# Performance work log

Hardware: AMD Instinct MI355X
Metric: run time of the kernel (lower is better)

Reference implementation:

```python
import jax, jax.numpy as jnp
import numpy as np

N_NODES = 100000
D = 128            # node feature dim == hidden_units[0]
N_EDGES = 640000
BN_EPS = 1e-3      # keras BatchNormalization default epsilon


def setup_inputs() -> dict:
    key = jax.random.key(0)
    ks = jax.random.split(key, 12)
    node_repr = jax.random.normal(ks[0], (N_NODES, D), dtype=jnp.float32)
    edges = jax.random.randint(ks[1], (2, N_EDGES), 0, N_NODES, dtype=jnp.int64)
    # ffn_prepare: BN(D) -> Dense(D, gelu)   (dropout inactive at inference)
    bn1_gamma = jax.random.normal(ks[2], (D,), dtype=jnp.float32) * 0.1 + 1.0
    bn1_beta = jax.random.normal(ks[3], (D,), dtype=jnp.float32) * 0.1
    bn1_mean = jax.random.normal(ks[4], (D,), dtype=jnp.float32) * 0.1
    bn1_var = jax.random.uniform(ks[5], (D,), dtype=jnp.float32) + 0.5
    W1 = jax.random.normal(ks[6], (D, D), dtype=jnp.float32) / np.sqrt(D)
    b1 = jnp.zeros((D,), dtype=jnp.float32)
    # update_fn: BN(2D) -> Dense(D, gelu)
    bn2_gamma = jax.random.normal(ks[7], (2 * D,), dtype=jnp.float32) * 0.1 + 1.0
    bn2_beta = jax.random.normal(ks[8], (2 * D,), dtype=jnp.float32) * 0.1
    bn2_mean = jax.random.normal(ks[9], (2 * D,), dtype=jnp.float32) * 0.1
    bn2_var = jax.random.uniform(ks[10], (2 * D,), dtype=jnp.float32) + 0.5
    W2 = jax.random.normal(ks[11], (2 * D, D), dtype=jnp.float32) / np.sqrt(2 * D)
    b2 = jnp.zeros((D,), dtype=jnp.float32)
    return dict(node_repr=node_repr, edges=edges,
                bn1_gamma=bn1_gamma, bn1_beta=bn1_beta, bn1_mean=bn1_mean, bn1_var=bn1_var,
                W1=W1, b1=b1,
                bn2_gamma=bn2_gamma, bn2_beta=bn2_beta, bn2_mean=bn2_mean, bn2_var=bn2_var,
                W2=W2, b2=b2)


def _bn(x, gamma, beta, mean, var):
    # inference-mode batch norm
    return (x - mean) * jax.lax.rsqrt(var + BN_EPS) * gamma + beta


def reference(node_repr, edges, bn1_gamma, bn1_beta, bn1_mean, bn1_var, W1, b1,
              bn2_gamma, bn2_beta, bn2_mean, bn2_var, W2, b2):
    num_nodes = node_repr.shape[0]
    node_indices, neighbour_indices = edges[0], edges[1]
    # gather neighbour features: [E, D]
    neigh = node_repr[neighbour_indices]
    # prepare FFN (BN -> dropout(identity at eval) -> Dense + exact gelu)
    msg = jax.nn.gelu(_bn(neigh, bn1_gamma, bn1_beta, bn1_mean, bn1_var) @ W1 + b1,
                      approximate=False)
    # unsorted_segment_mean: sum / count, empty segments -> 0 (TF semantics)
    sums = jax.ops.segment_sum(msg, node_indices, num_segments=num_nodes)
    cnt = jax.ops.segment_sum(jnp.ones((edges.shape[1],), msg.dtype), node_indices,
                              num_segments=num_nodes)
    agg = sums / jnp.maximum(cnt, 1.0)[:, None]
    # update FFN on concat [node_repr, agg]: [N, 2D] -> [N, D]
    h = jnp.concatenate([node_repr, agg], axis=1)
    out = jax.nn.gelu(_bn(h, bn2_gamma, bn2_beta, bn2_mean, bn2_var) @ W2 + b2,
                      approximate=False)
    return out
```

## Files before the change

### kernel.cpp

```cpp
#include <hip/hip_runtime.h>

#define NN 100000
#define DD 128
#define EE 640000
#define BN_EPS 1e-3f
#define NBLK 391
#define NTILE 6250
#define EPB 1637
#define FFN1_BLKS 782
#define FFN2_BLKS 768

typedef __bf16 bf16x8 __attribute__((ext_vector_type(8)));
typedef float f32x4 __attribute__((ext_vector_type(4)));

#define W1F_OFF 0u
#define W2F_OFF 32768u
#define B1F_OFF 98304u
#define B2F_OFF 98816u
#define T_OFF   99328u
#define OFFS_OFF 26099328u
#define ELIST_OFF 26899328u
#define CNTG_OFF ELIST_OFF
#define BOFS_OFF (ELIST_OFF + 611524u)
#define BSUM_OFF 29459328u
#define AGG_OFF 29464576u
#define XB_OFF  55064576u

__device__ __forceinline__ float gelu_fast(float x) {
    float x3 = x * x * x;
    float z2 = 1.5957691216057308f * x + 0.07135481627002407f * x3;
    return x / (1.0f + __expf(-z2));
}

__global__ __launch_bounds__(256) void prep_kernel(
    const float* __restrict__ g1, const float* __restrict__ be1,
    const float* __restrict__ m1, const float* __restrict__ v1,
    const float* __restrict__ W1, const float* __restrict__ b1,
    const float* __restrict__ g2, const float* __restrict__ be2,
    const float* __restrict__ m2, const float* __restrict__ v2,
    const float* __restrict__ W2, const float* __restrict__ b2,
    const int* __restrict__ edges,
    __bf16* __restrict__ W1f, __bf16* __restrict__ W2f,
    float* __restrict__ b1f, float* __restrict__ b2f,
    int* __restrict__ cntg)
{
    const int blk = blockIdx.x;
    const int t = threadIdx.x;
    if (blk < 64) {
        const int w = (blk * 256 + t) >> 6;
        const int lane = t & 63;
        if (w < 128) {
            float acc = 0.f;
            for (int k = lane; k < 128; k += 64) {
                float s = g1[k] * rsqrtf(v1[k] + BN_EPS);
                float sh = be1[k] - m1[k] * s;
                acc += sh * W1[k * 128 + w];
            }
#pragma unroll
            for (int off = 32; off > 0; off >>= 1) acc += __shfl_down(acc, off);
            if (lane == 0) b1f[w] = acc + b1[w];
        } else {
            const int n = w - 128;
            float acc = 0.f;
            for (int k = lane; k < 256; k += 64) {
                float s = g2[k] * rsqrtf(v2[k] + BN_EPS);
                float sh = be2[k] - m2[k] * s;
                acc += sh * W2[k * 128 + n];
            }
#pragma unroll
            for (int off = 32; off > 0; off >>= 1) acc += __shfl_down(acc, off);
            if (lane == 0) b2f[n] = acc + b2[n];
        }
    } else if (blk < 256) {
        int tid = (blk - 64) * 256 + t;
        if (tid < 16384) {
            int idx = tid;
            int i = idx & 7, l = (idx >> 3) & 63, nt = (idx >> 9) & 7, kt = idx >> 12;
            int k = kt * 32 + (l >> 4) * 8 + i;
            int n = nt * 16 + (l & 15);
            float s = g1[k] * rsqrtf(v1[k] + BN_EPS);
            W1f[idx] = (__bf16)(s * W1[k * 128 + n]);
        } else {
            int idx = tid - 16384;
            int i = idx & 7, l = (idx >> 3) & 63, nt = (idx >> 9) & 7, kt = idx >> 12;
            int n = nt * 16 + (l & 15);
            int row;
            if (kt < 4) {
                row = kt * 32 + (l >> 4) * 8 + i;
            } else {
                int q = (kt - 4) * 32 + (l >> 4) * 8 + i;
                row = 128 + ((q & 7) * 16 + (q >> 3));
            }
            float s = g2[row] * rsqrtf(v2[row] + BN_EPS);
            W2f[idx] = (__bf16)(s * W2[row * 128 + n]);
        }
    } else {
        __shared__ int cnt[NBLK];
        const int k = blk - 256;
        for (int b = t; b < NBLK; b += 256) cnt[b] = 0;
        __syncthreads();
        const int e0 = k * EPB, e1 = min(e0 + EPB, EE);
        for (int e = e0 + t; e < e1; e += 256)
            atomicAdd(&cnt[edges[e] >> 8], 1);
        __syncthreads();
        for (int b = t; b < NBLK; b += 256) cntg[k * NBLK + b] = cnt[b];
    }
}

__global__ __launch_bounds__(256) void sortb_kernel(const int* __restrict__ cntg,
                                                    int* __restrict__ bofs,
                                                    int* __restrict__ bsum)
{
    const int b = blockIdx.x, t = threadIdx.x;
    __shared__ int sp[256];
    int ia = 2 * t, ib = 2 * t + 1;
    int va = (ia < NBLK) ? cntg[ia * NBLK + b] : 0;
    int vb = (ib < NBLK) ? cntg[ib * NBLK + b] : 0;
    sp[t] = va + vb;
    __syncthreads();
    for (int off = 1; off < 256; off <<= 1) {
        int tmp = (t >= off) ? sp[t - off] : 0;
        __syncthreads();
        sp[t] += tmp;
        __syncthreads();
    }
    int pexcl = sp[t] - (va + vb);
    if (ia < NBLK) bofs[b * NBLK + ia] = pexcl;
    if (ib < NBLK) bofs[b * NBLK + ib] = pexcl + va;
    if (t == 255) bsum[b] = sp[255];
}

__global__ __launch_bounds__(256) void sortc_kernel(const int* __restrict__ edges,
                                                    const int* __restrict__ bsum,
                                                    const int* __restrict__ bofs,
                                                    int* __restrict__ pairbuf)
{
    __shared__ int sp[256];
    __shared__ int cur[NBLK];
    const int k = blockIdx.x, t = threadIdx.x;
    int ia = 2 * t, ib = 2 * t + 1;
    int va = (ia < NBLK) ? bsum[ia] : 0;
    int vb = (ib < NBLK) ? bsum[ib] : 0;
    sp[t] = va + vb;
    __syncthreads();
    for (int off = 1; off < 256; off <<= 1) {
        int tmp = (t >= off) ? sp[t - off] : 0;
        __syncthreads();
        sp[t] += tmp;
        __syncthreads();
    }
    int pexcl = sp[t] - (va + vb);
    if (ia < NBLK) cur[ia] = pexcl + bofs[ia * NBLK + k];
    if (ib < NBLK) cur[ib] = pexcl + va + bofs[ib * NBLK + k];
    __syncthreads();
    const int e0 = k * EPB, e1 = min(e0 + EPB, EE);
    for (int e = e0 + t; e < e1; e += 256) {
        int dst = edges[e];
        int src = edges[EE + e];
        int pos = atomicAdd(&cur[dst >> 8], 1);
        pairbuf[pos] = (src << 8) | (dst & 255);
    }
}

__global__ __launch_bounds__(256) void p2_ffn1_kernel(
    const int* __restrict__ bsum, const int* __restrict__ pairbuf,
    int* __restrict__ elist, int* __restrict__ offs,
    const float* __restrict__ X, const __bf16* __restrict__ W1f,
    const float* __restrict__ b1f, __bf16* __restrict__ T,
    __bf16* __restrict__ Xb)
{
    __shared__ __bf16 sW[16384];
    const int t = threadIdx.x;
    if (blockIdx.x < NBLK) {
        int* sArr = (int*)sW;
        int* cur  = sArr + 256;
        int* red  = sArr + 512;
        const int b = blockIdx.x;
        int part = 0;
        for (int i = t; i < b; i += 256) part += bsum[i];
#pragma unroll
        for (int off = 32; off > 0; off >>= 1) part += __shfl_down(part, off);
        if ((t & 63) == 0) red[t >> 6] = part;
        cur[t] = 0;
        __syncthreads();
        const int start = red[0] + red[1] + red[2] + red[3];
        const int end = start + bsum[b];
        for (int e = start + t; e < end; e += 256)
            atomicAdd(&cur[pairbuf[e] & 255], 1);
        __syncthreads();
        int v = cur[t];
        sArr[t] = v;
        __syncthreads();
        for (int off = 1; off < 256; off <<= 1) {
            int tmp = (t >= off) ? sArr[t - off] : 0;
            __syncthreads();
            sArr[t] += tmp;
            __syncthreads();
        }
        int ex = sArr[t] - v + start;
        const int node = b * 256 + t;
        if (node <= NN) offs[node] = ex;
        __syncthreads();
        cur[t] = ex;
        __syncthreads();
        for (int e = start + t; e < end; e += 256) {
            int item = pairbuf[e];
            int pos = atomicAdd(&cur[item & 255], 1);
            elist[pos] = item >> 8;
        }
        return;
    }
#pragma unroll
    for (int i = 0; i < 8; ++i) {
        int ch = i * 256 + t;
        *(bf16x8*)(sW + ch * 8) = *(const bf16x8*)(W1f + (size_t)ch * 8);
    }
    __syncthreads();

    const int wave = t >> 6;
    const int lane = t & 63;
    const int c = lane & 15, kh = lane >> 4;
    const int tbase = (blockIdx.x - NBLK) * 8;
    const int tile0 = tbase + wave;
    const int tile1 = tbase + 4 + wave;

    float bias[8];
#pragma unroll
    for (int nt = 0; nt < 8; ++nt) bias[nt] = b1f[nt * 16 + c];

    f32x4 r0[4], r1[4], s0[4], s1[4];
    bf16x8 af[4];

    if (tile0 < NTILE) {
        const float* xr = X + (size_t)(tile0 * 16 + c) * DD + kh * 8;
#pragma unroll
        for (int q = 0; q < 4; ++q) {
            r0[q] = *(const f32x4*)(xr + q * 32);
            r1[q] = *(const f32x4*)(xr + q * 32 + 4);
        }
    }
    if (tile1 < NTILE) {
        const float* xr = X + (size_t)(tile1 * 16 + c) * DD + kh * 8;
#pragma unroll
        for (int q = 0; q < 4; ++q) {
            s0[q] = *(const f32x4*)(xr + q * 32);
            s1[q] = *(const f32x4*)(xr + q * 32 + 4);
        }
    }

    if (tile0 < NTILE) {
        const size_t rowb = (size_t)(tile0 * 16 + c) * DD;
#pragma unroll
        for (int kt = 0; kt < 4; ++kt) {
            bf16x8 fa;
#pragma unroll
            for (int i = 0; i < 4; ++i) { fa[i] = (__bf16)r0[kt][i]; fa[4 + i] = (__bf16)r1[kt][i]; }
            af[kt] = fa;
            *(bf16x8*)(Xb + rowb + kt * 32 + kh * 8) = fa;
        }
        f32x4 acc[8] = {};
#pragma unroll
        for (int kt = 0; kt < 4; ++kt)
#pragma unroll
            for (int nt = 0; nt < 8; ++nt) {
                bf16x8 bfr = *(const bf16x8*)(sW + ((kt * 8 + nt) * 64 + lane) * 8);
                acc[nt] = __builtin_amdgcn_mfma_f32_16x16x32_bf16(af[kt], bfr, acc[nt], 0, 0, 0);
            }
#pragma unroll
        for (int r = 0; r < 4; ++r) {
            int row = tile0 * 16 + kh * 4 + r;
            bf16x8 o;
#pragma unroll
            for (int nt = 0; nt < 8; ++nt)
                o[nt] = (__bf16)gelu_fast(acc[nt][r] + bias[nt]);
            *(bf16x8*)(T + (size_t)row * DD + c * 8) = o;
        }
    }
    if (tile1 < NTILE) {
        const size_t rowb = (size_t)(tile1 * 16 + c) * DD;
#pragma unroll
        for (int kt = 0; kt < 4; ++kt) {
            bf16x8 fa;
#pragma unroll
            for (int i = 0; i < 4; ++i) { fa[i] = (__bf16)s0[kt][i]; fa[4 + i] = (__bf16)s1[kt][i]; }
            af[kt] = fa;
            *(bf16x8*)(Xb + rowb + kt * 32 + kh * 8) = fa;
        }
        f32x4 acc[8] = {};
#pragma unroll
        for (int kt = 0; kt < 4; ++kt)
#pragma unroll
            for (int nt = 0; nt < 8; ++nt) {
                bf16x8 bfr = *(const bf16x8*)(sW + ((kt * 8 + nt) * 64 + lane) * 8);
                acc[nt] = __builtin_amdgcn_mfma_f32_16x16x32_bf16(af[kt], bfr, acc[nt], 0, 0, 0);
            }
#pragma unroll
        for (int r = 0; r < 4; ++r) {
            int row = tile1 * 16 + kh * 4 + r;
            bf16x8 o;
#pragma unroll
            for (int nt = 0; nt < 8; ++nt)
                o[nt] = (__bf16)gelu_fast(acc[nt][r] + bias[nt]);
            *(bf16x8*)(T + (size_t)row * DD + c * 8) = o;
        }
    }
}

__global__ __launch_bounds__(256) void agg_kernel(
    const __bf16* __restrict__ T, const int* __restrict__ offs,
    const int* __restrict__ elist, __bf16* __restrict__ Agg)
{
    int t = blockIdx.x * 256 + threadIdx.x;
    int node = t >> 4, j = t & 15;
    if (node >= NN) return;
    const int lane = threadIdx.x & 63;
    const int gbase = lane & 48;
    const int beg = offs[node];
    const int end = offs[node + 1];
    const int d = end - beg;
    float acc[8] = {};
    for (int eb = beg; eb < end; eb += 16) {
        int me = eb + (lane & 15);
        int sv = (me < end) ? elist[me] : 0;
        int cnt = min(end - eb, 16);
        int i = 0;
        for (; i + 3 < cnt; i += 4) {
            int s0 = __shfl(sv, gbase + i);
            int s1 = __shfl(sv, gbase + i + 1);
            int s2 = __shfl(sv, gbase + i + 2);
            int s3 = __shfl(sv, gbase + i + 3);
            bf16x8 v0 = *(const bf16x8*)(T + (size_t)s0 * DD + j * 8);
            bf16x8 v1 = *(const bf16x8*)(T + (size_t)s1 * DD + j * 8);
            bf16x8 v2 = *(const bf16x8*)(T + (size_t)s2 * DD + j * 8);
            bf16x8 v3 = *(const bf16x8*)(T + (size_t)s3 * DD + j * 8);
#pragma unroll
            for (int q = 0; q < 8; ++q)
                acc[q] += ((float)v0[q] + (float)v1[q]) + ((float)v2[q] + (float)v3[q]);
        }
        for (; i < cnt; ++i) {
            int s0 = __shfl(sv, gbase + i);
            bf16x8 v0 = *(const bf16x8*)(T + (size_t)s0 * DD + j * 8);
#pragma unroll
            for (int q = 0; q < 8; ++q) acc[q] += (float)v0[q];
        }
    }
    const float inv = 1.0f / fmaxf((float)d, 1.0f);
    bf16x8 o;
#pragma unroll
    for (int q = 0; q < 8; ++q) o[q] = (__bf16)(acc[q] * inv);
    *(bf16x8*)(Agg + (size_t)node * DD + j * 8) = o;
}

#define FFN2_LOAD(TT, XA, GA)                                              \
    {                                                                      \
        const size_t rb = (size_t)((TT) * 16 + c) * DD + kh * 8;           \
        _Pragma("unroll")                                                  \
        for (int q = 0; q < 4; ++q) {                                      \
            XA[q] = *(const bf16x8*)(Xb + rb + q * 32);                    \
            GA[q] = *(const bf16x8*)(Agg + rb + q * 32);                   \
        }                                                                  \
    }

#define FFN2_COMP(TT, XA, GA)                                              \
    {                                                                      \
        f32x4 acc0 = {}, acc1 = {};                                        \
        _Pragma("unroll")                                                  \
        for (int kt = 0; kt < 4; ++kt) {                                   \
            acc0 = __builtin_amdgcn_mfma_f32_16x16x32_bf16(XA[kt], Bf[kt][0], acc0, 0, 0, 0); \
            acc1 = __builtin_amdgcn_mfma_f32_16x16x32_bf16(XA[kt], Bf[kt][1], acc1, 0, 0, 0); \
        }                                                                  \
        _Pragma("unroll")                                                  \
        for (int kt = 0; kt < 4; ++kt) {                                   \
            acc0 = __builtin_amdgcn_mfma_f32_16x16x32_bf16(GA[kt], Bf[4 + kt][0], acc0, 0, 0, 0); \
            acc1 = __builtin_amdgcn_mfma_f32_16x16x32_bf16(GA[kt], Bf[4 + kt][1], acc1, 0, 0, 0); \
        }                                                                  \
        _Pragma("unroll")                                                  \
        for (int r = 0; r < 4; ++r) {                                      \
            int row = (TT) * 16 + kh * 4 + r;                              \
            out[(size_t)row * DD + (w * 2) * 16 + c] = gelu_fast(acc0[r] + bias0); \
            out[(size_t)row * DD + (w * 2 + 1) * 16 + c] = gelu_fast(acc1[r] + bias1); \
        }                                                                  \
    }

__global__ __launch_bounds__(256) void ffn2_kernel(
    const __bf16* __restrict__ Xb, const __bf16* __restrict__ Agg,
    const __bf16* __restrict__ W2f, const float* __restrict__ b2f,
    float* __restrict__ out)
{
    const int w = threadIdx.x >> 6;
    const int lane = threadIdx.x & 63;
    const int c = lane & 15, kh = lane >> 4;
    const int G = gridDim.x;

    bf16x8 Bf[8][2];
#pragma unroll
    for (int kt = 0; kt < 8; ++kt) {
        Bf[kt][0] = *(const bf16x8*)(W2f + ((size_t)((kt * 8 + w * 2) * 64 + lane)) * 8);
        Bf[kt][1] = *(const bf16x8*)(W2f + ((size_t)((kt * 8 + w * 2 + 1) * 64 + lane)) * 8);
    }
    const float bias0 = b2f[(w * 2) * 16 + c];
    const float bias1 = b2f[(w * 2 + 1) * 16 + c];

    int tile = blockIdx.x;
    if (tile >= NTILE) return;
    bf16x8 xa[4], ga[4], xb2[4], gb[4];
    FFN2_LOAD(tile, xa, ga);
    while (true) {
        int t2 = tile + G;
        if (t2 < NTILE) FFN2_LOAD(t2, xb2, gb);
        FFN2_COMP(tile, xa, ga);
        if (t2 >= NTILE) break;
        int t3 = t2 + G;
        if (t3 < NTILE) FFN2_LOAD(t3, xa, ga);
        FFN2_COMP(t2, xb2, gb);
        if (t3 >= NTILE) break;
        tile = t3;
    }
}

extern "C" void kernel_launch(void* const* d_in, const int* in_sizes, int n_in,
                              void* d_out, int out_size, void* d_ws, size_t ws_size,
                              hipStream_t stream) {
    const float* node_repr = (const float*)d_in[0];
    const int*   edges     = (const int*)d_in[1];
    const float* g1 = (const float*)d_in[2];
    const float* be1 = (const float*)d_in[3];
    const float* m1 = (const float*)d_in[4];
    const float* v1 = (const float*)d_in[5];
    const float* W1 = (const float*)d_in[6];
    const float* b1 = (const float*)d_in[7];
    const float* g2 = (const float*)d_in[8];
    const float* be2 = (const float*)d_in[9];
    const float* m2 = (const float*)d_in[10];
    const float* v2 = (const float*)d_in[11];
    const float* W2 = (const float*)d_in[12];
    const float* b2 = (const float*)d_in[13];

    char* ws = (char*)d_ws;
    __bf16* W1f = (__bf16*)(ws + W1F_OFF);
    __bf16* W2f = (__bf16*)(ws + W2F_OFF);
    float* b1f = (float*)(ws + B1F_OFF);
    float* b2f = (float*)(ws + B2F_OFF);
    __bf16* T  = (__bf16*)(ws + T_OFF);
    int* offs  = (int*)(ws + OFFS_OFF);
    int* elist = (int*)(ws + ELIST_OFF);
    int* cntg  = (int*)(ws + CNTG_OFF);
    int* bofs  = (int*)(ws + BOFS_OFF);
    int* bsum  = (int*)(ws + BSUM_OFF);
    __bf16* Agg = (__bf16*)(ws + AGG_OFF);
    int* pairbuf = (int*)(ws + AGG_OFF);
    __bf16* Xb = (__bf16*)(ws + XB_OFF);
    float* out = (float*)d_out;

    hipLaunchKernelGGL(prep_kernel, dim3(256 + NBLK), dim3(256), 0, stream,
                       g1, be1, m1, v1, W1, b1, g2, be2, m2, v2, W2, b2,
                       edges, W1f, W2f, b1f, b2f, cntg);

    hipLaunchKernelGGL(sortb_kernel, dim3(NBLK), dim3(256), 0, stream, cntg, bofs, bsum);

    hipLaunchKernelGGL(sortc_kernel, dim3(NBLK), dim3(256), 0, stream,
                       edges, bsum, bofs, pairbuf);

    hipLaunchKernelGGL(p2_ffn1_kernel, dim3(NBLK + FFN1_BLKS), dim3(256), 0, stream,
                       bsum, pairbuf, elist, offs, node_repr, W1f, b1f, T, Xb);

    hipLaunchKernelGGL(agg_kernel, dim3((NN * 16 + 255) / 256), dim3(256), 0, stream,
                       T, offs, elist, Agg);

    hipLaunchKernelGGL(ffn2_kernel, dim3(FFN2_BLKS), dim3(256), 0, stream,
                       Xb, Agg, W2f, b2f, out);
}
```

Baseline: 104.5 us.

## Fuse neighbour aggregation into the update FFN kernel via shared memory

Merges the segment-mean aggregation kernel into the second FFN kernel. Each block gathers and averages the neighbour rows for its 16-node tile, stages the bf16 result in a swizzled shared-memory tile, and feeds it straight into the MFMA matmul. This removes the Agg round trip through global memory and one kernel launch. In exchange the gather loop becomes a simple serial per-edge loop without the unrolled shuffle batching, and it adds two block barriers per tile, which may limit how much memory-level parallelism the gather can expose.

After: 117.7 us. +12.7%, slower.

```diff
diff --git a/kernel.cpp b/kernel.cpp
--- a/kernel.cpp
+++ b/kernel.cpp
@@ -8,7 +8,7 @@
 #define NTILE 6250
 #define EPB 1637
 #define FFN1_BLKS 782
-#define FFN2_BLKS 768
+#define AF2_BLKS 1024
 
 typedef __bf16 bf16x8 __attribute__((ext_vector_type(8)));
 typedef float f32x4 __attribute__((ext_vector_type(4)));
@@ -306,91 +306,16 @@
     }
 }
 
-__global__ __launch_bounds__(256) void agg_kernel(
-    const __bf16* __restrict__ T, const int* __restrict__ offs,
-    const int* __restrict__ elist, __bf16* __restrict__ Agg)
-{
-    int t = blockIdx.x * 256 + threadIdx.x;
-    int node = t >> 4, j = t & 15;
-    if (node >= NN) return;
-    const int lane = threadIdx.x & 63;
-    const int gbase = lane & 48;
-    const int beg = offs[node];
-    const int end = offs[node + 1];
-    const int d = end - beg;
-    float acc[8] = {};
-    for (int eb = beg; eb < end; eb += 16) {
-        int me = eb + (lane & 15);
-        int sv = (me < end) ? elist[me] : 0;
-        int cnt = min(end - eb, 16);
-        int i = 0;
-        for (; i + 3 < cnt; i += 4) {
-            int s0 = __shfl(sv, gbase + i);
-            int s1 = __shfl(sv, gbase + i + 1);
-            int s2 = __shfl(sv, gbase + i + 2);
-            int s3 = __shfl(sv, gbase + i + 3);
-            bf16x8 v0 = *(const bf16x8*)(T + (size_t)s0 * DD + j * 8);
-            bf16x8 v1 = *(const bf16x8*)(T + (size_t)s1 * DD + j * 8);
-            bf16x8 v2 = *(const bf16x8*)(T + (size_t)s2 * DD + j * 8);
-            bf16x8 v3 = *(const bf16x8*)(T + (size_t)s3 * DD + j * 8);
-#pragma unroll
-            for (int q = 0; q < 8; ++q)
-                acc[q] += ((float)v0[q] + (float)v1[q]) + ((float)v2[q] + (float)v3[q]);
-        }
-        for (; i < cnt; ++i) {
-            int s0 = __shfl(sv, gbase + i);
-            bf16x8 v0 = *(const bf16x8*)(T + (size_t)s0 * DD + j * 8);
-#pragma unroll
-            for (int q = 0; q < 8; ++q) acc[q] += (float)v0[q];
-        }
-    }
-    const float inv = 1.0f / fmaxf((float)d, 1.0f);
-    bf16x8 o;
-#pragma unroll
-    for (int q = 0; q < 8; ++q) o[q] = (__bf16)(acc[q] * inv);
-    *(bf16x8*)(Agg + (size_t)node * DD + j * 8) = o;
-}
-
-#define FFN2_LOAD(TT, XA, GA)                                              \
-    {                                                                      \
-        const size_t rb = (size_t)((TT) * 16 + c) * DD + kh * 8;           \
-        _Pragma("unroll")                                                  \
-        for (int q = 0; q < 4; ++q) {                                      \
-            XA[q] = *(const bf16x8*)(Xb + rb + q * 32);                    \
-            GA[q] = *(const bf16x8*)(Agg + rb + q * 32);                   \
-        }                                                                  \
-    }
-
-#define FFN2_COMP(TT, XA, GA)                                              \
-    {                                                                      \
-        f32x4 acc0 = {}, acc1 = {};                                        \
-        _Pragma("unroll")                                                  \
-        for (int kt = 0; kt < 4; ++kt) {                                   \
-            acc0 = __builtin_amdgcn_mfma_f32_16x16x32_bf16(XA[kt], Bf[kt][0], acc0, 0, 0, 0); \
-            acc1 = __builtin_amdgcn_mfma_f32_16x16x32_bf16(XA[kt], Bf[kt][1], acc1, 0, 0, 0); \
-        }                                                                  \
-        _Pragma("unroll")                                                  \
-        for (int kt = 0; kt < 4; ++kt) {                                   \
-            acc0 = __builtin_amdgcn_mfma_f32_16x16x32_bf16(GA[kt], Bf[4 + kt][0], acc0, 0, 0, 0); \
-            acc1 = __builtin_amdgcn_mfma_f32_16x16x32_bf16(GA[kt], Bf[4 + kt][1], acc1, 0, 0, 0); \
-        }                                                                  \
-        _Pragma("unroll")                                                  \
-        for (int r = 0; r < 4; ++r) {                                      \
-            int row = (TT) * 16 + kh * 4 + r;                              \
-            out[(size_t)row * DD + (w * 2) * 16 + c] = gelu_fast(acc0[r] + bias0); \
-            out[(size_t)row * DD + (w * 2 + 1) * 16 + c] = gelu_fast(acc1[r] + bias1); \
-        }                                                                  \
-    }
-
-__global__ __launch_bounds__(256) void ffn2_kernel(
-    const __bf16* __restrict__ Xb, const __bf16* __restrict__ Agg,
+__global__ __launch_bounds__(256) void agg_ffn2_kernel(
+    const __bf16* __restrict__ Xb, const __bf16* __restrict__ T,
+    const int* __restrict__ offs, const int* __restrict__ elist,
     const __bf16* __restrict__ W2f, const float* __restrict__ b2f,
     float* __restrict__ out)
 {
+    __shared__ __bf16 sAgg[16 * 128];
     const int w = threadIdx.x >> 6;
     const int lane = threadIdx.x & 63;
     const int c = lane & 15, kh = lane >> 4;
-    const int G = gridDim.x;
 
     bf16x8 Bf[8][2];
 #pragma unroll
@@ -401,20 +326,58 @@
     const float bias0 = b2f[(w * 2) * 16 + c];
     const float bias1 = b2f[(w * 2 + 1) * 16 + c];
 
-    int tile = blockIdx.x;
-    if (tile >= NTILE) return;
-    bf16x8 xa[4], ga[4], xb2[4], gb[4];
-    FFN2_LOAD(tile, xa, ga);
-    while (true) {
-        int t2 = tile + G;
-        if (t2 < NTILE) FFN2_LOAD(t2, xb2, gb);
-        FFN2_COMP(tile, xa, ga);
-        if (t2 >= NTILE) break;
-        int t3 = t2 + G;
-        if (t3 < NTILE) FFN2_LOAD(t3, xa, ga);
-        FFN2_COMP(t2, xb2, gb);
-        if (t3 >= NTILE) break;
-        tile = t3;
+    for (int tile = blockIdx.x; tile < NTILE; tile += gridDim.x) {
+        bf16x8 xa[4];
+        const size_t rb = (size_t)(tile * 16 + c) * DD + kh * 8;
+#pragma unroll
+        for (int q = 0; q < 4; ++q)
+            xa[q] = *(const bf16x8*)(Xb + rb + q * 32);
+
+        {
+            const int arow = w * 4 + kh;
+            const int node = tile * 16 + arow;
+            const int j = c;
+            const int beg = offs[node], end = offs[node + 1];
+            float acc[8] = {};
+            for (int e = beg; e < end; ++e) {
+                int src = elist[e];
+                bf16x8 v = *(const bf16x8*)(T + (size_t)src * DD + j * 8);
+#pragma unroll
+                for (int q = 0; q < 8; ++q) acc[q] += (float)v[q];
+            }
+            const float inv = 1.0f / fmaxf((float)(end - beg), 1.0f);
+            bf16x8 o;
+#pragma unroll
+            for (int q = 0; q < 8; ++q) o[q] = (__bf16)(acc[q] * inv);
+            *(bf16x8*)(sAgg + arow * 128 + ((j ^ (arow & 7)) * 8)) = o;
+        }
+        __syncthreads();
+
+        bf16x8 ga[4];
+#pragma unroll
+        for (int kt = 0; kt < 4; ++kt) {
+            int jj = kt * 4 + kh;
+            ga[kt] = *(const bf16x8*)(sAgg + c * 128 + ((jj ^ (c & 7)) * 8));
+        }
+
+        f32x4 acc0 = {}, acc1 = {};
+#pragma unroll
+        for (int kt = 0; kt < 4; ++kt) {
+            acc0 = __builtin_amdgcn_mfma_f32_16x16x32_bf16(xa[kt], Bf[kt][0], acc0, 0, 0, 0);
+            acc1 = __builtin_amdgcn_mfma_f32_16x16x32_bf16(xa[kt], Bf[kt][1], acc1, 0, 0, 0);
+        }
+#pragma unroll
+        for (int kt = 0; kt < 4; ++kt) {
+            acc0 = __builtin_amdgcn_mfma_f32_16x16x32_bf16(ga[kt], Bf[4 + kt][0], acc0, 0, 0, 0);
+            acc1 = __builtin_amdgcn_mfma_f32_16x16x32_bf16(ga[kt], Bf[4 + kt][1], acc1, 0, 0, 0);
+        }
+#pragma unroll
+        for (int r = 0; r < 4; ++r) {
+            int row = tile * 16 + kh * 4 + r;
+            out[(size_t)row * DD + (w * 2) * 16 + c] = gelu_fast(acc0[r] + bias0);
+            out[(size_t)row * DD + (w * 2 + 1) * 16 + c] = gelu_fast(acc1[r] + bias1);
+        }
+        __syncthreads();
     }
 }
 
@@ -447,7 +410,6 @@
     int* cntg  = (int*)(ws + CNTG_OFF);
     int* bofs  = (int*)(ws + BOFS_OFF);
     int* bsum  = (int*)(ws + BSUM_OFF);
-    __bf16* Agg = (__bf16*)(ws + AGG_OFF);
     int* pairbuf = (int*)(ws + AGG_OFF);
     __bf16* Xb = (__bf16*)(ws + XB_OFF);
     float* out = (float*)d_out;
@@ -464,9 +426,6 @@
     hipLaunchKernelGGL(p2_ffn1_kernel, dim3(NBLK + FFN1_BLKS), dim3(256), 0, stream,
                        bsum, pairbuf, elist, offs, node_repr, W1f, b1f, T, Xb);
 
-    hipLaunchKernelGGL(agg_kernel, dim3((NN * 16 + 255) / 256), dim3(256), 0, stream,
-                       T, offs, elist, Agg);
-
-    hipLaunchKernelGGL(ffn2_kernel, dim3(FFN2_BLKS), dim3(256), 0, stream,
-                       Xb, Agg, W2f, b2f, out);
-}
+    hipLaunchKernelGGL(agg_ffn2_kernel, dim3(AF2_BLKS), dim3(256), 0, stream,
+                       Xb, T, offs, elist, W2f, b2f, out);
+}
```
